# Optimization experiments

Hardware: AMD Instinct MI355X
Metric: run time of the kernel (lower is better)

The kernel has to match this reference:

```python
import jax, jax.numpy as jnp
import numpy as np
import math

B, I, H = 8192, 1024, 1024

def _uniform(key, shape, lo, hi):
    return jax.random.uniform(key, shape, dtype=jnp.float32, minval=lo, maxval=hi)

def setup_inputs() -> dict:
    key = jax.random.key(0)
    ks = jax.random.split(key, 14)
    bound = math.sqrt(1.0 / H)
    lo, hi = -bound, bound
    x = jax.random.normal(ks[0], (B, I), dtype=jnp.float32)
    hid = jax.random.normal(ks[1], (B, H), dtype=jnp.float32)
    # stacked params for gates [r, z, n]
    wx = jnp.stack([_uniform(ks[2 + i], (I, H), lo, hi) for i in range(3)])   # [3, I, H]
    wh = jnp.stack([_uniform(ks[5 + i], (H, H), lo, hi) for i in range(3)])   # [3, H, H]
    bx = jnp.stack([_uniform(ks[8 + i], (H,), lo, hi) for i in range(3)])     # [3, H]
    bh = jnp.stack([_uniform(ks[11 + i], (H,), lo, hi) for i in range(3)])    # [3, H]
    return {"x": x, "hid": hid, "wx": wx, "wh": wh, "bx": bx, "bh": bh}

def reference(x, hid, wx, wh, bx, bh):
    # Fused gate projections: one big matmul per source instead of 3 small ones.
    gx = jnp.einsum('bi,gih->bgh', x, wx) + bx[None]        # [B, 3, H]
    gh = jnp.einsum('bh,ghk->bgk', hid, wh) + bh[None]      # [B, 3, H]
    r = jax.nn.sigmoid(gx[:, 0] + gh[:, 0])
    z = jax.nn.sigmoid(gx[:, 1] + gh[:, 1])
    n = jnp.tanh(gx[:, 2] + r * gh[:, 2])
    next_hid = (1.0 - z) * n + z * hid
    return next_hid
```

## Files before the change

kernel.cpp:

```cpp
#include <hip/hip_runtime.h>
#include <hip/hip_bf16.h>

typedef __hip_bfloat16 bf16;
typedef unsigned short u16;
typedef __attribute__((ext_vector_type(8))) short bf16x8;
typedef __attribute__((ext_vector_type(4))) float f32x4;
typedef __attribute__((ext_vector_type(8))) unsigned short u16x8;

#define KD 1024
#define HD 1024
#define BSZ 8192
#define BM 128
#define BN 64
#define BK 32

#define WS_XB 12582912
#define WS_HB 29360128
#define WS_NEED 46137344ULL

__device__ __forceinline__ u16 f2b(float f) {
    return __builtin_bit_cast(u16, __float2bfloat16(f));
}

__device__ __forceinline__ void gload16(const void* g, u16* smem, int lds_byte_off) {
    __builtin_amdgcn_global_load_lds(
        (const __attribute__((address_space(1))) void*)g,
        (__attribute__((address_space(3))) void*)((char*)smem + lds_byte_off),
        16, 0, 0);
}

__global__ __launch_bounds__(256) void convert_xh(
    const float* __restrict__ x, const float* __restrict__ h,
    u16* __restrict__ xb, u16* __restrict__ hb)
{
    size_t off = ((size_t)blockIdx.x * 256 + threadIdx.x) * 8;
    float4 a0 = *(const float4*)(x + off);
    float4 a1 = *(const float4*)(x + off + 4);
    float4 b0 = *(const float4*)(h + off);
    float4 b1 = *(const float4*)(h + off + 4);
    u16x8 vx, vh;
    vx[0]=f2b(a0.x); vx[1]=f2b(a0.y); vx[2]=f2b(a0.z); vx[3]=f2b(a0.w);
    vx[4]=f2b(a1.x); vx[5]=f2b(a1.y); vx[6]=f2b(a1.z); vx[7]=f2b(a1.w);
    vh[0]=f2b(b0.x); vh[1]=f2b(b0.y); vh[2]=f2b(b0.z); vh[3]=f2b(b0.w);
    vh[4]=f2b(b1.x); vh[5]=f2b(b1.y); vh[6]=f2b(b1.z); vh[7]=f2b(b1.w);
    *(u16x8*)(xb + off) = vx;
    *(u16x8*)(hb + off) = vh;
}

__global__ __launch_bounds__(256) void transpose_w(
    const float* __restrict__ wx, const float* __restrict__ wh, u16* __restrict__ wt)
{
    __shared__ u16 tile[64][65];
    const int g = blockIdx.z;
    const float* src = (g < 3) ? (wx + (size_t)g * KD * HD) : (wh + (size_t)(g - 3) * KD * HD);
    u16* dst = wt + (size_t)g * KD * HD;
    const int r0 = blockIdx.y * 64;
    const int c0 = blockIdx.x * 64;
    const int t = threadIdx.x;

    #pragma unroll
    for (int r = 0; r < 2; r++) {
        int idx = r * 256 + t;
        int row = idx >> 3, cc = idx & 7;
        const float* p = src + (size_t)(r0 + row) * HD + c0 + cc * 8;
        #pragma unroll
        for (int e = 0; e < 8; e++) tile[row][cc * 8 + e] = f2b(p[e]);
    }
    __syncthreads();
    #pragma unroll
    for (int r = 0; r < 2; r++) {
        int idx = r * 256 + t;
        int nrow = idx >> 3, kc = idx & 7;
        u16x8 v;
        #pragma unroll
        for (int e = 0; e < 8; e++) v[e] = tile[kc * 8 + e][nrow];
        *(u16x8*)(dst + (size_t)(c0 + nrow) * KD + r0 + kc * 8) = v;
    }
}

__device__ __forceinline__ void gru_epilogue(
    f32x4 (&acc)[4][4][2], const float* __restrict__ bxf, const float* __restrict__ bhf,
    const float* __restrict__ hidf, float* __restrict__ outf,
    int m0, int n0, int wm, int wn, int quad, int c16)
{
    float bR[2], bZ[2], bXN[2], bHN[2];
    #pragma unroll
    for (int j = 0; j < 2; j++) {
        int col = n0 + wn * 32 + j * 16 + c16;
        bR[j]  = bxf[col]          + bhf[col];
        bZ[j]  = bxf[HD + col]     + bhf[HD + col];
        bXN[j] = bxf[2 * HD + col];
        bHN[j] = bhf[2 * HD + col];
    }
    #pragma unroll
    for (int i = 0; i < 4; i++)
        #pragma unroll
        for (int j = 0; j < 2; j++) {
            int col = n0 + wn * 32 + j * 16 + c16;
            #pragma unroll
            for (int r = 0; r < 4; r++) {
                int row = m0 + wm * 64 + i * 16 + quad * 4 + r;
                size_t idx = (size_t)row * HD + col;
                float vr = acc[0][i][j][r] + bR[j];
                vr = 1.f / (1.f + __expf(-vr));
                float vz = acc[1][i][j][r] + bZ[j];
                vz = 1.f / (1.f + __expf(-vz));
                float vn = (acc[2][i][j][r] + bXN[j]) + vr * (acc[3][i][j][r] + bHN[j]);
                float e2 = __expf(2.f * vn);
                vn = 1.f - 2.f / (e2 + 1.f);
                float o = (1.f - vz) * vn + vz * hidf[idx];
                outf[idx] = o;
            }
        }
}

__device__ __forceinline__ void kstep_stage(
    const u16* gx0, const u16* gx1, const u16* gh0, const u16* gh1,
    const u16* gw0, u16* smem, int bufb, int ldsl)
{
    gload16(gx0, smem, bufb + ldsl);
    gload16(gx1, smem, bufb + 4096 + ldsl);
    gload16(gh0, smem, bufb + 8192 + ldsl);
    gload16(gh1, smem, bufb + 12288 + ldsl);
    #pragma unroll
    for (int g = 0; g < 6; g++)
        gload16(gw0 + (size_t)g * KD * HD, smem, bufb + 16384 + g * 4096 + ldsl);
}

__device__ __forceinline__ void kstep_compute(
    const u16* sm, f32x4 (&acc)[4][4][2], int wm, int wn, int quad, int c16)
{
    bf16x8 ax[4], ah[4];
    #pragma unroll
    for (int i = 0; i < 4; i++) {
        int ml = wm * 64 + i * 16 + c16;
        ax[i] = *(const bf16x8*)&sm[ml * BK + quad * 8];
        ah[i] = *(const bf16x8*)&sm[4096 + ml * BK + quad * 8];
    }
    #pragma unroll
    for (int p = 0; p < 3; p++) {
        bf16x8 bwx[2], bwh[2];
        #pragma unroll
        for (int j = 0; j < 2; j++) {
            int nl = wn * 32 + j * 16 + c16;
            bwx[j] = *(const bf16x8*)&sm[8192 + p * 2048       + nl * BK + quad * 8];
            bwh[j] = *(const bf16x8*)&sm[8192 + (p + 3) * 2048 + nl * BK + quad * 8];
        }
        #pragma unroll
        for (int i = 0; i < 4; i++)
            #pragma unroll
            for (int j = 0; j < 2; j++) {
                if (p < 2) {
                    acc[p][i][j] = __builtin_amdgcn_mfma_f32_16x16x32_bf16(ax[i], bwx[j], acc[p][i][j], 0, 0, 0);
                    acc[p][i][j] = __builtin_amdgcn_mfma_f32_16x16x32_bf16(ah[i], bwh[j], acc[p][i][j], 0, 0, 0);
                } else {
                    acc[2][i][j] = __builtin_amdgcn_mfma_f32_16x16x32_bf16(ax[i], bwx[j], acc[2][i][j], 0, 0, 0);
                    acc[3][i][j] = __builtin_amdgcn_mfma_f32_16x16x32_bf16(ah[i], bwh[j], acc[3][i][j], 0, 0, 0);
                }
            }
    }
}

__global__ __launch_bounds__(256, 2) void gru_fused_fast(
    const u16* __restrict__ xb, const u16* __restrict__ hb,
    const u16* __restrict__ wt,
    const float* __restrict__ bxf, const float* __restrict__ bhf,
    const float* __restrict__ hidf, float* __restrict__ outf)
{
    __shared__ u16 smem[40960];
    const int t    = threadIdx.x;
    const int lane = t & 63;
    const int w    = t >> 6;
    const int wm   = w >> 1, wn = w & 1;
    const int quad = lane >> 4;
    const int c16  = lane & 15;
    const int lin  = blockIdx.x;
    const int nblk = (lin & 7) * 2 + ((lin >> 3) & 1);
    const int mblk = lin >> 4;
    const int m0   = mblk * BM;
    const int n0   = nblk * BN;

    const int row4 = t >> 2;
    const int e8   = (t & 3) * 8;
    const u16* gx0 = xb + (size_t)(m0 + row4) * KD + e8;
    const u16* gx1 = gx0 + (size_t)64 * KD;
    const u16* gh0 = hb + (size_t)(m0 + row4) * KD + e8;
    const u16* gh1 = gh0 + (size_t)64 * KD;
    const u16* gw0 = wt + (size_t)(n0 + row4) * KD + e8;
    const int ldsl = w * 1024;

    f32x4 acc[4][4][2];
    #pragma unroll
    for (int a = 0; a < 4; a++)
        #pragma unroll
        for (int i = 0; i < 4; i++)
            #pragma unroll
            for (int j = 0; j < 2; j++)
                acc[a][i][j] = (f32x4){0.f, 0.f, 0.f, 0.f};

    const int NT = KD / BK;

    kstep_stage(gx0, gx1, gh0, gh1, gw0, smem, 0, ldsl);
    gx0 += BK; gx1 += BK; gh0 += BK; gh1 += BK; gw0 += BK;
    __syncthreads();

    for (int tt = 0; tt < NT - 1; ++tt) {
        kstep_stage(gx0, gx1, gh0, gh1, gw0, smem, ((tt + 1) & 1) * 40960, ldsl);
        gx0 += BK; gx1 += BK; gh0 += BK; gh1 += BK; gw0 += BK;
        kstep_compute(smem + (tt & 1) * 20480, acc, wm, wn, quad, c16);
        __syncthreads();
    }
    kstep_compute(smem + 20480, acc, wm, wn, quad, c16);

    gru_epilogue(acc, bxf, bhf, hidf, outf, m0, n0, wm, wn, quad, c16);
}

__global__ __launch_bounds__(256, 2) void gru_fused_slow(
    const float* __restrict__ xf, const float* __restrict__ hf,
    const u16* __restrict__ wt,
    const float* __restrict__ bxf, const float* __restrict__ bhf,
    float* __restrict__ outf)
{
    __shared__ u16 smem[20480];
    const int t    = threadIdx.x;
    const int lane = t & 63;
    const int w    = t >> 6;
    const int wm   = w >> 1, wn = w & 1;
    const int quad = lane >> 4;
    const int c16  = lane & 15;
    const int lin  = blockIdx.x;
    const int nblk = (lin & 7) * 2 + ((lin >> 3) & 1);
    const int mblk = lin >> 4;
    const int m0   = mblk * BM;
    const int n0   = nblk * BN;
    const int row4 = t >> 2;
    const int e8   = (t & 3) * 8;
    const u16* gw0 = wt + (size_t)(n0 + row4) * KD + e8;
    const int ldsl = w * 1024;

    f32x4 acc[4][4][2];
    #pragma unroll
    for (int a = 0; a < 4; a++)
        #pragma unroll
        for (int i = 0; i < 4; i++)
            #pragma unroll
            for (int j = 0; j < 2; j++)
                acc[a][i][j] = (f32x4){0.f, 0.f, 0.f, 0.f};

    for (int k0 = 0; k0 < KD; k0 += BK) {
        #pragma unroll
        for (int g = 0; g < 6; g++)
            gload16(gw0 + (size_t)g * KD * HD, smem, 16384 + g * 4096 + ldsl);
        gw0 += BK;
        #pragma unroll
        for (int s = 0; s < 2; s++) {
            size_t gidx = (size_t)(m0 + s * 64 + row4) * KD + k0 + e8;
            const float* px = xf + gidx;
            const float* ph = hf + gidx;
            u16x8 vx, vh;
            #pragma unroll
            for (int e = 0; e < 8; e++) { vx[e] = f2b(px[e]); vh[e] = f2b(ph[e]); }
            *(u16x8*)&smem[s * 2048 + t * 8] = vx;
            *(u16x8*)&smem[4096 + s * 2048 + t * 8] = vh;
        }
        __syncthreads();
        kstep_compute(smem, acc, wm, wn, quad, c16);
        __syncthreads();
    }

    gru_epilogue(acc, bxf, bhf, hf, outf, m0, n0, wm, wn, quad, c16);
}

extern "C" void kernel_launch(void* const* d_in, const int* in_sizes, int n_in,
                              void* d_out, int out_size, void* d_ws, size_t ws_size,
                              hipStream_t stream) {
    const float* x   = (const float*)d_in[0];
    const float* hid = (const float*)d_in[1];
    const float* wx  = (const float*)d_in[2];
    const float* wh  = (const float*)d_in[3];
    const float* bx  = (const float*)d_in[4];
    const float* bh  = (const float*)d_in[5];
    float* out = (float*)d_out;

    char* ws = (char*)d_ws;
    u16* wt = (u16*)ws;
    u16* xb = (u16*)(ws + WS_XB);
    u16* hb = (u16*)(ws + WS_HB);

    dim3 tgrid(HD / 64, KD / 64, 6);
    transpose_w<<<tgrid, 256, 0, stream>>>(wx, wh, wt);

    if (ws_size >= WS_NEED) {
        convert_xh<<<4096, 256, 0, stream>>>(x, hid, xb, hb);
        gru_fused_fast<<<1024, 256, 0, stream>>>(xb, hb, wt, bx, bh, hid, out);
    } else {
        gru_fused_slow<<<1024, 256, 0, stream>>>(x, hid, wt, bx, bh, out);
    }
}
```

Before: 243.6 us.

## Load fp32 activations directly into registers and drop separate bf16 conversion pass

Removes the convert_xh pre-pass and its workspace buffers. Each wave now loads its fp32 x/h fragments straight from global memory into registers, converts them to bf16 in-register, and prefetches the next k-step while the MFMAs run. Only the weight tiles are still staged through LDS, with an XOR swizzle added to cut bank conflicts, which also shrinks the shared-memory footprint. In exchange, the fp32 activation loads carry twice the bytes per k-step and are not shared across the two N-waves, so each row's A data is fetched redundantly, and register pressure rises.

```diff
diff --git a/kernel.cpp b/kernel.cpp
--- a/kernel.cpp
+++ b/kernel.cpp
@@ -1,7 +1,6 @@
 #include <hip/hip_runtime.h>
 #include <hip/hip_bf16.h>
 
-typedef __hip_bfloat16 bf16;
 typedef unsigned short u16;
 typedef __attribute__((ext_vector_type(8))) short bf16x8;
 typedef __attribute__((ext_vector_type(4))) float f32x4;
@@ -9,14 +8,10 @@
 
 #define KD 1024
 #define HD 1024
-#define BSZ 8192
 #define BM 128
 #define BN 64
 #define BK 32
-
-#define WS_XB 12582912
-#define WS_HB 29360128
-#define WS_NEED 46137344ULL
+#define NT (KD / BK)
 
 __device__ __forceinline__ u16 f2b(float f) {
     return __builtin_bit_cast(u16, __float2bfloat16(f));
@@ -27,24 +22,6 @@
         (const __attribute__((address_space(1))) void*)g,
         (__attribute__((address_space(3))) void*)((char*)smem + lds_byte_off),
         16, 0, 0);
-}
-
-__global__ __launch_bounds__(256) void convert_xh(
-    const float* __restrict__ x, const float* __restrict__ h,
-    u16* __restrict__ xb, u16* __restrict__ hb)
-{
-    size_t off = ((size_t)blockIdx.x * 256 + threadIdx.x) * 8;
-    float4 a0 = *(const float4*)(x + off);
-    float4 a1 = *(const float4*)(x + off + 4);
-    float4 b0 = *(const float4*)(h + off);
-    float4 b1 = *(const float4*)(h + off + 4);
-    u16x8 vx, vh;
-    vx[0]=f2b(a0.x); vx[1]=f2b(a0.y); vx[2]=f2b(a0.z); vx[3]=f2b(a0.w);
-    vx[4]=f2b(a1.x); vx[5]=f2b(a1.y); vx[6]=f2b(a1.z); vx[7]=f2b(a1.w);
-    vh[0]=f2b(b0.x); vh[1]=f2b(b0.y); vh[2]=f2b(b0.z); vh[3]=f2b(b0.w);
-    vh[4]=f2b(b1.x); vh[5]=f2b(b1.y); vh[6]=f2b(b1.z); vh[7]=f2b(b1.w);
-    *(u16x8*)(xb + off) = vx;
-    *(u16x8*)(hb + off) = vh;
 }
 
 __global__ __launch_bounds__(256) void transpose_w(
@@ -114,37 +91,28 @@
         }
 }
 
-__device__ __forceinline__ void kstep_stage(
-    const u16* gx0, const u16* gx1, const u16* gh0, const u16* gh1,
-    const u16* gw0, u16* smem, int bufb, int ldsl)
-{
-    gload16(gx0, smem, bufb + ldsl);
-    gload16(gx1, smem, bufb + 4096 + ldsl);
-    gload16(gh0, smem, bufb + 8192 + ldsl);
-    gload16(gh1, smem, bufb + 12288 + ldsl);
-    #pragma unroll
-    for (int g = 0; g < 6; g++)
-        gload16(gw0 + (size_t)g * KD * HD, smem, bufb + 16384 + g * 4096 + ldsl);
-}
-
-__device__ __forceinline__ void kstep_compute(
-    const u16* sm, f32x4 (&acc)[4][4][2], int wm, int wn, int quad, int c16)
-{
-    bf16x8 ax[4], ah[4];
-    #pragma unroll
-    for (int i = 0; i < 4; i++) {
-        int ml = wm * 64 + i * 16 + c16;
-        ax[i] = *(const bf16x8*)&sm[ml * BK + quad * 8];
-        ah[i] = *(const bf16x8*)&sm[4096 + ml * BK + quad * 8];
-    }
+__device__ __forceinline__ bf16x8 cvt8(const float4& a, const float4& b) {
+    bf16x8 r;
+    r[0] = (short)f2b(a.x); r[1] = (short)f2b(a.y);
+    r[2] = (short)f2b(a.z); r[3] = (short)f2b(a.w);
+    r[4] = (short)f2b(b.x); r[5] = (short)f2b(b.y);
+    r[6] = (short)f2b(b.z); r[7] = (short)f2b(b.w);
+    return r;
+}
+
+__device__ __forceinline__ void kstep_mfma(
+    const u16* sm, const bf16x8 (&ax)[4], const bf16x8 (&ah)[4],
+    f32x4 (&acc)[4][4][2], int wn, int quad, int c16)
+{
     #pragma unroll
     for (int p = 0; p < 3; p++) {
         bf16x8 bwx[2], bwh[2];
         #pragma unroll
         for (int j = 0; j < 2; j++) {
             int nl = wn * 32 + j * 16 + c16;
-            bwx[j] = *(const bf16x8*)&sm[8192 + p * 2048       + nl * BK + quad * 8];
-            bwh[j] = *(const bf16x8*)&sm[8192 + (p + 3) * 2048 + nl * BK + quad * 8];
+            int slot = (quad ^ ((nl >> 1) & 3)) * 8;
+            bwx[j] = *(const bf16x8*)&sm[p * 2048       + nl * BK + slot];
+            bwh[j] = *(const bf16x8*)&sm[(p + 3) * 2048 + nl * BK + slot];
         }
         #pragma unroll
         for (int i = 0; i < 4; i++)
@@ -161,13 +129,13 @@
     }
 }
 
-__global__ __launch_bounds__(256, 2) void gru_fused_fast(
-    const u16* __restrict__ xb, const u16* __restrict__ hb,
+__global__ __launch_bounds__(256, 2) void gru_fused(
+    const float* __restrict__ xf, const float* __restrict__ hf,
     const u16* __restrict__ wt,
     const float* __restrict__ bxf, const float* __restrict__ bhf,
-    const float* __restrict__ hidf, float* __restrict__ outf)
-{
-    __shared__ u16 smem[40960];
+    float* __restrict__ outf)
+{
+    __shared__ u16 smem[24576];
     const int t    = threadIdx.x;
     const int lane = t & 63;
     const int w    = t >> 6;
@@ -181,13 +149,12 @@
     const int n0   = nblk * BN;
 
     const int row4 = t >> 2;
-    const int e8   = (t & 3) * 8;
-    const u16* gx0 = xb + (size_t)(m0 + row4) * KD + e8;
-    const u16* gx1 = gx0 + (size_t)64 * KD;
-    const u16* gh0 = hb + (size_t)(m0 + row4) * KD + e8;
-    const u16* gh1 = gh0 + (size_t)64 * KD;
-    const u16* gw0 = wt + (size_t)(n0 + row4) * KD + e8;
+    const int e8s  = ((t & 3) ^ ((t >> 3) & 3)) * 8;
+    const u16* gw0 = wt + (size_t)(n0 + row4) * KD + e8s;
     const int ldsl = w * 1024;
+
+    const float* pax = xf + (size_t)(m0 + wm * 64 + c16) * KD + quad * 8;
+    const float* pah = hf + (size_t)(m0 + wm * 64 + c16) * KD + quad * 8;
 
     f32x4 acc[4][4][2];
     #pragma unroll
@@ -198,74 +165,51 @@
             for (int j = 0; j < 2; j++)
                 acc[a][i][j] = (f32x4){0.f, 0.f, 0.f, 0.f};
 
-    const int NT = KD / BK;
-
-    kstep_stage(gx0, gx1, gh0, gh1, gw0, smem, 0, ldsl);
-    gx0 += BK; gx1 += BK; gh0 += BK; gh1 += BK; gw0 += BK;
+    float4 afx[4][2], afh[4][2];
+
+    auto loadA = [&](int koff) {
+        #pragma unroll
+        for (int i = 0; i < 4; i++) {
+            const float* px = pax + (size_t)i * 16 * KD + koff;
+            const float* ph = pah + (size_t)i * 16 * KD + koff;
+            afx[i][0] = *(const float4*)px;
+            afx[i][1] = *(const float4*)(px + 4);
+            afh[i][0] = *(const float4*)ph;
+            afh[i][1] = *(const float4*)(ph + 4);
+        }
+    };
+    auto stageW = [&](const u16* gw, int bufb) {
+        #pragma unroll
+        for (int g = 0; g < 6; g++)
+            gload16(gw + (size_t)g * KD * HD, smem, bufb + g * 4096 + ldsl);
+    };
+
+    loadA(0);
+    stageW(gw0, 0);
+    gw0 += BK;
     __syncthreads();
 
     for (int tt = 0; tt < NT - 1; ++tt) {
-        kstep_stage(gx0, gx1, gh0, gh1, gw0, smem, ((tt + 1) & 1) * 40960, ldsl);
-        gx0 += BK; gx1 += BK; gh0 += BK; gh1 += BK; gw0 += BK;
-        kstep_compute(smem + (tt & 1) * 20480, acc, wm, wn, quad, c16);
+        bf16x8 ax[4], ah[4];
+        #pragma unroll
+        for (int i = 0; i < 4; i++) {
+            ax[i] = cvt8(afx[i][0], afx[i][1]);
+            ah[i] = cvt8(afh[i][0], afh[i][1]);
+        }
+        loadA((tt + 1) * BK);
+        stageW(gw0, ((tt + 1) & 1) * 24576);
+        gw0 += BK;
+        kstep_mfma(smem + (tt & 1) * 12288, ax, ah, acc, wn, quad, c16);
         __syncthreads();
     }
-    kstep_compute(smem + 20480, acc, wm, wn, quad, c16);
-
-    gru_epilogue(acc, bxf, bhf, hidf, outf, m0, n0, wm, wn, quad, c16);
-}
-
-__global__ __launch_bounds__(256, 2) void gru_fused_slow(
-    const float* __restrict__ xf, const float* __restrict__ hf,
-    const u16* __restrict__ wt,
-    const float* __restrict__ bxf, const float* __restrict__ bhf,
-    float* __restrict__ outf)
-{
-    __shared__ u16 smem[20480];
-    const int t    = threadIdx.x;
-    const int lane = t & 63;
-    const int w    = t >> 6;
-    const int wm   = w >> 1, wn = w & 1;
-    const int quad = lane >> 4;
-    const int c16  = lane & 15;
-    const int lin  = blockIdx.x;
-    const int nblk = (lin & 7) * 2 + ((lin >> 3) & 1);
-    const int mblk = lin >> 4;
-    const int m0   = mblk * BM;
-    const int n0   = nblk * BN;
-    const int row4 = t >> 2;
-    const int e8   = (t & 3) * 8;
-    const u16* gw0 = wt + (size_t)(n0 + row4) * KD + e8;
-    const int ldsl = w * 1024;
-
-    f32x4 acc[4][4][2];
-    #pragma unroll
-    for (int a = 0; a < 4; a++)
-        #pragma unroll
-        for (int i = 0; i < 4; i++)
-            #pragma unroll
-            for (int j = 0; j < 2; j++)
-                acc[a][i][j] = (f32x4){0.f, 0.f, 0.f, 0.f};
-
-    for (int k0 = 0; k0 < KD; k0 += BK) {
-        #pragma unroll
-        for (int g = 0; g < 6; g++)
-            gload16(gw0 + (size_t)g * KD * HD, smem, 16384 + g * 4096 + ldsl);
-        gw0 += BK;
-        #pragma unroll
-        for (int s = 0; s < 2; s++) {
-            size_t gidx = (size_t)(m0 + s * 64 + row4) * KD + k0 + e8;
-            const float* px = xf + gidx;
-            const float* ph = hf + gidx;
-            u16x8 vx, vh;
-            #pragma unroll
-            for (int e = 0; e < 8; e++) { vx[e] = f2b(px[e]); vh[e] = f2b(ph[e]); }
-            *(u16x8*)&smem[s * 2048 + t * 8] = vx;
-            *(u16x8*)&smem[4096 + s * 2048 + t * 8] = vh;
-        }
-        __syncthreads();
-        kstep_compute(smem, acc, wm, wn, quad, c16);
-        __syncthreads();
+    {
+        bf16x8 ax[4], ah[4];
+        #pragma unroll
+        for (int i = 0; i < 4; i++) {
+            ax[i] = cvt8(afx[i][0], afx[i][1]);
+            ah[i] = cvt8(afh[i][0], afh[i][1]);
+        }
+        kstep_mfma(smem + 12288, ax, ah, acc, wn, quad, c16);
     }
 
     gru_epilogue(acc, bxf, bhf, hf, outf, m0, n0, wm, wn, quad, c16);
@@ -282,18 +226,9 @@
     const float* bh  = (const float*)d_in[5];
     float* out = (float*)d_out;
 
-    char* ws = (char*)d_ws;
-    u16* wt = (u16*)ws;
-    u16* xb = (u16*)(ws + WS_XB);
-    u16* hb = (u16*)(ws + WS_HB);
+    u16* wt = (u16*)d_ws;
 
     dim3 tgrid(HD / 64, KD / 64, 6);
     transpose_w<<<tgrid, 256, 0, stream>>>(wx, wh, wt);
-
-    if (ws_size >= WS_NEED) {
-        convert_xh<<<4096, 256, 0, stream>>>(x, hid, xb, hb);
-        gru_fused_fast<<<1024, 256, 0, stream>>>(xb, hb, wt, bx, bh, hid, out);
-    } else {
-        gru_fused_slow<<<1024, 256, 0, stream>>>(x, hid, wt, bx, bh, out);
-    }
-}
+    gru_fused<<<1024, 256, 0, stream>>>(x, hid, wt, bx, bh, out);
+}
```

After: 386.7 us. 58.8% more time.
